# Optimization experiments

Hardware: AMD Instinct MI355X
Metric: run time of the kernel (lower is better)

Reference implementation:

```python
import math
import jax, jax.numpy as jnp
import numpy as np

THETA_BINS = 8
PHI_BINS = 8
BLOCK_SIZE = 15
MAX_PHI = math.pi
DVOL = 64  # input volume is DVOL^3
EPS = 2.220446049250313e-16  # sys.float_info.epsilon


def _sobel_weight():
    # Fixed (3,1,3,3,3) central-difference kernels: channel 0 = d/dz, 1 = d/dy, 2 = d/dx
    w = np.zeros((3, 1, 3, 3, 3), np.float32)
    w[0, 0, 0, 1, 1] = -1.0; w[0, 0, 2, 1, 1] = 1.0  # s_z
    w[1, 0, 1, 0, 1] = -1.0; w[1, 0, 1, 2, 1] = 1.0  # s_y
    w[2, 0, 1, 1, 0] = -1.0; w[2, 0, 1, 1, 2] = 1.0  # s_x
    return jnp.asarray(w)


def setup_inputs() -> dict:
    key = jax.random.key(0)
    x = jax.random.normal(key, (DVOL, DVOL, DVOL), dtype=jnp.float32)
    return {"x": x, "weight": _sobel_weight()}


def reference(x, weight):
    offset = BLOCK_SIZE // 2 + 1  # 8; output spatial = d + 2*offset - 2
    xb = x.astype(jnp.float32)[None, None]  # (1,1,d,h,w)
    out = jax.lax.conv_general_dilated(
        xb, weight, window_strides=(1, 1, 1),
        padding=[(offset, offset)] * 3,
        dimension_numbers=("NCDHW", "OIDHW", "NCDHW"))[0]  # (3, D, H, W)

    mag = jnp.sqrt(jnp.sum(out * out, axis=0))              # (D,H,W) frobenius over channel
    theta = jnp.arctan2(out[1], out[2])
    phi = jnp.arccos(out[0] / (mag + EPS))

    # NOTE: original code divides theta by max_phi_angle and scales by phi_bins (faithful)
    t_raw = theta / MAX_PHI * PHI_BINS
    p_raw = phi / MAX_PHI * PHI_BINS
    t_frac = t_raw - jnp.trunc(t_raw)  # torch.frac semantics
    p_frac = p_raw - jnp.trunc(p_raw)

    i0 = jnp.floor(t_raw).astype(jnp.int32) % THETA_BINS  # theta lower bin
    i1 = jnp.ceil(t_raw).astype(jnp.int32) % THETA_BINS   # theta upper bin
    i2 = jnp.floor(p_raw).astype(jnp.int32) % PHI_BINS    # phi lower bin
    i3 = jnp.ceil(p_raw).astype(jnp.int32) % PHI_BINS     # phi upper bin

    f0 = jnp.abs(t_frac); f1 = jnp.abs(1.0 - t_frac)
    f2 = jnp.abs(p_frac); f3 = jnp.abs(1.0 - p_frac)
    w0 = (f0 * f2) * mag  # scattered to (i0, i2) via scatter_ set
    w1 = (f0 * f3) * mag  # scatter_add at (i0, i3)
    w2 = (f1 * f2) * mag  # scatter_add at (i1, i2)

    # The torch scatter_/scatter_add_ chain (zero fill elsewhere, initial tensor zeros)
    # reduces exactly to three one-hot depositions per voxel; 4th add is absent
    # because the source forward is truncated after the third scatter_add_.
    tb = jnp.arange(THETA_BINS, dtype=jnp.int32)[:, None, None, None]  # (T,1,1,1)
    pb = jnp.arange(PHI_BINS, dtype=jnp.int32)[:, None, None, None]   # (P,1,1,1)
    t0 = (tb == i0).astype(mag.dtype)  # (T,D,H,W)
    t1 = (tb == i1).astype(mag.dtype)
    p2 = (pb == i2).astype(mag.dtype)  # (P,D,H,W)
    p3 = (pb == i3).astype(mag.dtype)

    out_plus_bins = (t0[:, None] * p2[None] * w0
                     + t0[:, None] * p3[None] * w1
                     + t1[:, None] * p2[None] * w2)  # (T,P,D,H,W)
    return out_plus_bins[None]  # (1, theta_bins, phi_bins, D, H, W)
```

## Files before the change

### kernel.cpp

```cpp
#include <hip/hip_runtime.h>
#include <math.h>


#define DVOL 64
#define S 78
#define S3 (S * S * S)

__device__ __forceinline__ float ldx(const float* __restrict__ x, int z, int y, int xx) {
    if ((unsigned)z < (unsigned)DVOL && (unsigned)y < (unsigned)DVOL && (unsigned)xx < (unsigned)DVOL)
        return x[(z * DVOL + y) * DVOL + xx];
    return 0.0f;
}

__global__ void __launch_bounds__(256) hog_scatter(const float* __restrict__ x,
                                                   float* __restrict__ out) {
#pragma clang fp contract(off)
    int idx = blockIdx.x * blockDim.x + threadIdx.x;
    if (idx >= S3) return;
    int ox = idx % S;
    int r  = idx / S;
    int oy = r % S;
    int oz = r / S;
    int ix = ox - 7, iy = oy - 7, iz = oz - 7;

    float gz = ldx(x, iz + 1, iy, ix) - ldx(x, iz - 1, iy, ix);
    float gy = ldx(x, iz, iy + 1, ix) - ldx(x, iz, iy - 1, ix);
    float gx = ldx(x, iz, iy, ix + 1) - ldx(x, iz, iy, ix - 1);

    float mag2 = (gz * gz + gy * gy) + gx * gx;
    float mag  = sqrtf(mag2);

    float wv0 = 0.0f, wv1 = 0.0f, wv2 = 0.0f;
    int b0 = -1, b1 = -1, b2 = -1;

    if (mag != 0.0f) {
        float theta = (float)atan2((double)gy, (double)gx);
        const float EPS32 = 2.220446049250313e-16f;
        float denom = mag + EPS32;
        float ratio = gz / denom;
        float phi = (float)acos((double)ratio);

        const float PI32 = 3.14159274101257324f;
        float t_raw = theta / PI32 * 8.0f;
        float p_raw = phi   / PI32 * 8.0f;

        float t_frac = t_raw - truncf(t_raw);
        float p_frac = p_raw - truncf(p_raw);

        int i0 = ((int)floorf(t_raw)) & 7;
        int i1 = ((int)ceilf (t_raw)) & 7;
        int i2 = ((int)floorf(p_raw)) & 7;
        int i3 = ((int)ceilf (p_raw)) & 7;

        float f0 = fabsf(t_frac), f1 = fabsf(1.0f - t_frac);
        float f2 = fabsf(p_frac), f3 = fabsf(1.0f - p_frac);
        wv0 = (f0 * f2) * mag;
        wv1 = (f0 * f3) * mag;
        wv2 = (f1 * f2) * mag;

        b0 = i0 * 8 + i2; b1 = i0 * 8 + i3; b2 = i1 * 8 + i2;
        if (b1 == b0) { wv0 = wv0 + wv1; b1 = -1; }
        if (b2 == b0) { wv0 = wv0 + wv2; b2 = -1; }
    }

    #pragma unroll
    for (int p = 0; p < 64; ++p) {
        float v = 0.0f;
        if (p == b0) v = wv0;
        if (p == b1) v = wv1;
        if (p == b2) v = wv2;
        out[(size_t)p * S3 + idx] = v;
    }
}

extern "C" void kernel_launch(void* const* d_in, const int* in_sizes, int n_in,
                              void* d_out, int out_size, void* d_ws, size_t ws_size,
                              hipStream_t stream) {
    const float* x = (const float*)d_in[0];
    float* out = (float*)d_out;

    const int threads = 256;
    const int blocks = (S3 + threads - 1) / threads;
    hog_scatter<<<blocks, threads, 0, stream>>>(x, out);
}
```

Before: 131.1 us.

## Process four voxels per thread with float4 stores and fast float trig

Each thread now handles four consecutive voxels and writes the 64 output planes as 16-byte float4 stores instead of scalar stores, which cuts the store instruction count on this write-bound kernel. The double-precision atan2 and acos are replaced by float atan2f/acosf, with a fallback to double only when the value lies within 1e-4 of a bin boundary, so the binning stays correct. Blocks shrink to 64 threads, and each thread holds more registers.

Result: no change. 131.3 us (+0.2%).

```diff
diff --git a/kernel.cpp b/kernel.cpp
--- a/kernel.cpp
+++ b/kernel.cpp
@@ -5,6 +5,7 @@
 #define DVOL 64
 #define S 78
 #define S3 (S * S * S)
+#define NQ (S3 / 4)
 
 __device__ __forceinline__ float ldx(const float* __restrict__ x, int z, int y, int xx) {
     if ((unsigned)z < (unsigned)DVOL && (unsigned)y < (unsigned)DVOL && (unsigned)xx < (unsigned)DVOL)
@@ -12,11 +13,10 @@
     return 0.0f;
 }
 
-__global__ void __launch_bounds__(256) hog_scatter(const float* __restrict__ x,
-                                                   float* __restrict__ out) {
+__device__ __forceinline__ void analyze(const float* __restrict__ x, int idx,
+                                        int& bo0, int& bo1, int& bo2,
+                                        float& wo0, float& wo1, float& wo2) {
 #pragma clang fp contract(off)
-    int idx = blockIdx.x * blockDim.x + threadIdx.x;
-    if (idx >= S3) return;
     int ox = idx % S;
     int r  = idx / S;
     int oy = r % S;
@@ -30,46 +30,74 @@
     float mag2 = (gz * gz + gy * gy) + gx * gx;
     float mag  = sqrtf(mag2);
 
-    float wv0 = 0.0f, wv1 = 0.0f, wv2 = 0.0f;
-    int b0 = -1, b1 = -1, b2 = -1;
+    bo0 = bo1 = bo2 = -1;
+    wo0 = wo1 = wo2 = 0.0f;
+    if (mag == 0.0f) return;
 
-    if (mag != 0.0f) {
-        float theta = (float)atan2((double)gy, (double)gx);
-        const float EPS32 = 2.220446049250313e-16f;
-        float denom = mag + EPS32;
-        float ratio = gz / denom;
-        float phi = (float)acos((double)ratio);
+    const float EPS32 = 2.220446049250313e-16f;
+    const float PI32  = 3.14159274101257324f;
+    float denom = mag + EPS32;
+    float ratio = gz / denom;
 
-        const float PI32 = 3.14159274101257324f;
-        float t_raw = theta / PI32 * 8.0f;
-        float p_raw = phi   / PI32 * 8.0f;
+    float theta = atan2f(gy, gx);
+    float phi   = acosf(ratio);
+    float t_raw = theta / PI32 * 8.0f;
+    float p_raw = phi   / PI32 * 8.0f;
 
-        float t_frac = t_raw - truncf(t_raw);
-        float p_frac = p_raw - truncf(p_raw);
+    float td = fabsf(t_raw - rintf(t_raw));
+    float pd = fabsf(p_raw - rintf(p_raw));
+    if (td < 1e-4f || pd < 1e-4f) {
+        theta = (float)atan2((double)gy, (double)gx);
+        phi   = (float)acos((double)ratio);
+        t_raw = theta / PI32 * 8.0f;
+        p_raw = phi   / PI32 * 8.0f;
+    }
 
-        int i0 = ((int)floorf(t_raw)) & 7;
-        int i1 = ((int)ceilf (t_raw)) & 7;
-        int i2 = ((int)floorf(p_raw)) & 7;
-        int i3 = ((int)ceilf (p_raw)) & 7;
+    float t_frac = t_raw - truncf(t_raw);
+    float p_frac = p_raw - truncf(p_raw);
 
-        float f0 = fabsf(t_frac), f1 = fabsf(1.0f - t_frac);
-        float f2 = fabsf(p_frac), f3 = fabsf(1.0f - p_frac);
-        wv0 = (f0 * f2) * mag;
-        wv1 = (f0 * f3) * mag;
-        wv2 = (f1 * f2) * mag;
+    int i0 = ((int)floorf(t_raw)) & 7;
+    int i1 = ((int)ceilf (t_raw)) & 7;
+    int i2 = ((int)floorf(p_raw)) & 7;
+    int i3 = ((int)ceilf (p_raw)) & 7;
 
-        b0 = i0 * 8 + i2; b1 = i0 * 8 + i3; b2 = i1 * 8 + i2;
-        if (b1 == b0) { wv0 = wv0 + wv1; b1 = -1; }
-        if (b2 == b0) { wv0 = wv0 + wv2; b2 = -1; }
-    }
+    float f0 = fabsf(t_frac), f1 = fabsf(1.0f - t_frac);
+    float f2 = fabsf(p_frac), f3 = fabsf(1.0f - p_frac);
+    float w0 = (f0 * f2) * mag;
+    float w1 = (f0 * f3) * mag;
+    float w2 = (f1 * f2) * mag;
+
+    int b0 = i0 * 8 + i2, b1 = i0 * 8 + i3, b2 = i1 * 8 + i2;
+    if (b1 == b0) { w0 = w0 + w1; b1 = -1; }
+    if (b2 == b0) { w0 = w0 + w2; b2 = -1; }
+
+    bo0 = b0; bo1 = b1; bo2 = b2;
+    wo0 = w0; wo1 = w1; wo2 = w2;
+}
+
+__global__ void __launch_bounds__(64) hog4(const float* __restrict__ x,
+                                           float4* __restrict__ out4) {
+    int t = blockIdx.x * 64 + threadIdx.x;
+    if (t >= NQ) return;
+    int base = t * 4;
+
+    int   b[4][3];
+    float w[4][3];
+    #pragma unroll
+    for (int v = 0; v < 4; ++v)
+        analyze(x, base + v, b[v][0], b[v][1], b[v][2], w[v][0], w[v][1], w[v][2]);
 
     #pragma unroll
     for (int p = 0; p < 64; ++p) {
-        float v = 0.0f;
-        if (p == b0) v = wv0;
-        if (p == b1) v = wv1;
-        if (p == b2) v = wv2;
-        out[(size_t)p * S3 + idx] = v;
+        float4 val = make_float4(0.0f, 0.0f, 0.0f, 0.0f);
+        #pragma unroll
+        for (int d = 0; d < 3; ++d) {
+            if (b[0][d] == p) val.x = w[0][d];
+            if (b[1][d] == p) val.y = w[1][d];
+            if (b[2][d] == p) val.z = w[2][d];
+            if (b[3][d] == p) val.w = w[3][d];
+        }
+        out4[(size_t)p * NQ + t] = val;
     }
 }
 
@@ -77,9 +105,9 @@
                               void* d_out, int out_size, void* d_ws, size_t ws_size,
                               hipStream_t stream) {
     const float* x = (const float*)d_in[0];
-    float* out = (float*)d_out;
+    float4* out4 = (float4*)d_out;
 
-    const int threads = 256;
-    const int blocks = (S3 + threads - 1) / threads;
-    hog_scatter<<<blocks, threads, 0, stream>>>(x, out);
+    const int threads = 64;
+    const int blocks = (NQ + threads - 1) / threads;
+    hog4<<<blocks, threads, 0, stream>>>(x, out4);
 }
```
